# Performance work log

Measured on AMD Instinct MI355X. Metric: run time of the kernel, lower is better.

## Reference

```python
import jax, jax.numpy as jnp
import numpy as np

# --- NAVAR dims (from init_kwargs) ---
ND, NS, NV, HID = 2, 4, 12, 16      # n_datasets, n_samples, n_variables, hidden_dim
GROUPS = ND * NS * NV               # 96 independent grouped-conv streams
K = 4                               # kernel_size
NBLOCKS = 3                         # dilated blocks, dilations 1,2,4
B, T = 8, 2048                      # batch, sequence length


def causal_conv(x, w, b, dilation, groups):
    """Grouped causal dilated 1D conv. x:(B,C,T), w:(O, C//groups, K), b:(O,)."""
    pad = (w.shape[-1] - 1) * dilation
    y = jax.lax.conv_general_dilated(
        x, w, window_strides=(1,), padding=[(pad, 0)],
        rhs_dilation=(dilation,),
        dimension_numbers=("NCH", "OIH", "NCH"),
        feature_group_count=groups,
    )
    return y + b[None, :, None]


def setup_inputs() -> dict:
    key = jax.random.key(0)
    ks = jax.random.split(key, 5)
    s = lambda fan_in: np.float32(1.0 / np.sqrt(fan_in))
    x = jax.random.normal(ks[0], (B, ND, NS, NV, T), dtype=jnp.float32)
    # grouped input conv: 1 -> HID channels per group
    w_in = jax.random.normal(ks[1], (GROUPS * HID, 1, K), dtype=jnp.float32) * s(K)
    b_in = jnp.zeros((GROUPS * HID,), jnp.float32)
    # dilated hidden blocks: HID -> HID per group
    w_h = jax.random.normal(ks[2], (NBLOCKS, GROUPS * HID, HID, K), dtype=jnp.float32) * s(HID * K)
    b_h = jnp.zeros((NBLOCKS, GROUPS * HID), jnp.float32)
    # grouped 1x1 output conv: HID -> NV contributions per group
    w_out = jax.random.normal(ks[3], (GROUPS * NV, HID, 1), dtype=jnp.float32) * s(HID)
    b_out = jnp.zeros((GROUPS * NV,), jnp.float32)
    # NAVAR additive biases (init 0.01 as in torch code)
    biases = jnp.full((1, ND, NS, NV, 1), 0.01, jnp.float32)
    return dict(x=x, w_in=w_in, b_in=b_in, w_h=w_h, b_h=b_h,
                w_out=w_out, b_out=b_out, biases=biases)


def reference(x, w_in, b_in, w_h, b_h, w_out, b_out, biases):
    batch = x.shape[0]
    h = x.reshape(batch, GROUPS, T)                       # (B, groups, T)
    h = jax.nn.relu(causal_conv(h, w_in, b_in, 1, GROUPS))
    for i in range(NBLOCKS):                              # fixed small loop over layers
        h = jax.nn.relu(causal_conv(h, w_h[i], b_h[i], 2 ** i, GROUPS))
    c = causal_conv(h, w_out, b_out, 1, GROUPS)           # (B, groups*NV, T)
    c = c.reshape(batch, ND, NS, NV, NV, T)               # (B, nd, ns, src, dst, T)
    prediction = c.sum(axis=-3) + biases                  # sum over source variables
    contributions = jnp.swapaxes(c, -2, -3)               # (B, nd, ns, dst, src, T)
    return prediction, contributions
```

## Files before the change

kernel.cpp:

```cpp
#include <hip/hip_runtime.h>

#define T_LEN   2048
#define BATCH   8
#define HIDDEN  16
#define KSZ     4
#define NVAR    12
#define NGROUPS 96

#define WOUT  104
#define WHALO 24
#define WPOS  128
#define WPAD  16
#define ROWCH 24
#define NBT   5

#define NWH  (3 * NGROUPS * HIDDEN * HIDDEN * KSZ)
#define NWO  (NGROUPS * HIDDEN * 32)

typedef __attribute__((ext_vector_type(8))) short bf16x8;
typedef __attribute__((ext_vector_type(4))) float f32x4;

__device__ __forceinline__ unsigned short f2bf(float x) {
    union { float f; unsigned u; } v; v.f = x;
    unsigned r = v.u + 0x7FFFu + ((v.u >> 16) & 1u);
    return (unsigned short)(r >> 16);
}

__device__ __forceinline__ unsigned cvtpk(float lo, float hi) {
    unsigned r;
    asm("v_cvt_pk_bf16_f32 %0, %1, %2" : "=v"(r) : "v"(lo), "v"(hi));
    return r;
}

__device__ __forceinline__ void lds_fence() {
    asm volatile("s_waitcnt lgkmcnt(0)" ::: "memory");
    __builtin_amdgcn_sched_barrier(0);
}

__global__ __launch_bounds__(256) void navar_pack(
        const float* __restrict__ w_h, const float* __restrict__ w_out,
        unsigned short* __restrict__ wp, unsigned short* __restrict__ wpo) {
    const int e = blockIdx.x * 256 + threadIdx.x;
    if (e < NWH) {
        const int k  = e & 63, row = e >> 6;
        const int kk = k >> 4, i = k & 15;
        wp[e] = f2bf(w_h[(row << 6) + i * 4 + kk]);
    } else {
        const int e2 = e - NWH;
        const int k = e2 & 31, m = (e2 >> 5) & 15, g = e2 >> 9;
        wpo[e2] = (k < 16 && m < 12) ? f2bf(w_out[(g * NVAR + m) * HIDDEN + k])
                                     : (unsigned short)0;
    }
}

template<int D, int NT>
__device__ __forceinline__ void mfma_layer(
        unsigned short (*hbw)[ROWCH],
        const bf16x8 a0, const bf16x8 a1, const f32x4 bias,
        int W0, int q, int c) {
    const int ch = (q & 1) * 8;
    const int d0 = (3 - (q >> 1)) * D;
    const int d1 = (1 - (q >> 1)) * D;

    f32x4 acc[NT];
    #pragma unroll
    for (int tt = 0; tt < NT; ++tt) {
        const int pos = tt * 16 + c;
        const bf16x8 b0 = *(const bf16x8*)&hbw[pos - d0][ch];
        const bf16x8 b1 = *(const bf16x8*)&hbw[pos - d1][ch];
        acc[tt] = bias;
        acc[tt] = __builtin_amdgcn_mfma_f32_16x16x32_bf16(a0, b0, acc[tt], 0, 0, 0);
        acc[tt] = __builtin_amdgcn_mfma_f32_16x16x32_bf16(a1, b1, acc[tt], 0, 0, 0);
    }
    asm volatile("" ::: "memory");
    #pragma unroll
    for (int tt = 0; tt < NT; ++tt) {
        const int pos = tt * 16 + c;
        const int tgp = W0 + pos - WHALO;
        uint2 pku;
        pku.x = cvtpk(fmaxf(acc[tt][0], 0.f), fmaxf(acc[tt][1], 0.f));
        pku.y = cvtpk(fmaxf(acc[tt][2], 0.f), fmaxf(acc[tt][3], 0.f));
        if (tgp < 0) { pku.x = 0u; pku.y = 0u; }
        *(uint2*)&hbw[pos][q * 4] = pku;
    }
}

__global__ __launch_bounds__(256, 5) void navar_main(
        const float* __restrict__ x,
        const float* __restrict__ w_in,  const float* __restrict__ b_in,
        const unsigned short* __restrict__ wp, const float* __restrict__ b_h,
        const unsigned short* __restrict__ wpo, const float* __restrict__ b_out,
        float* __restrict__ contrib) {
    __shared__ unsigned short hb[WPAD + 4 * WPOS][ROWCH];

    const int p    = threadIdx.x;
    const int wave = p >> 6, lane = p & 63;
    const int q    = lane >> 4, c = lane & 15;
    const int bt   = blockIdx.x % NBT;
    const int sg   = blockIdx.x / NBT;
    const int b    = sg / NGROUPS;
    const int g    = sg % NGROUPS;
    const int tw   = bt * 4 + wave;
    const int W0   = tw * WOUT;

    unsigned short (*hw)[ROWCH] =
        (unsigned short (*)[ROWCH])&hb[WPAD + wave * WPOS];

    const size_t wstep = (size_t)NGROUPS * HIDDEN * (HIDDEN * KSZ);
    const unsigned short* wr0 =
        wp + (size_t)(g * HIDDEN + c) * (HIDDEN * KSZ);
    bf16x8 A0[3], A1[3]; f32x4 BH[3];
    #pragma unroll
    for (int l = 0; l < 3; ++l) {
        A0[l] = *(const bf16x8*)(wr0 + l * wstep + q * 8);
        A1[l] = *(const bf16x8*)(wr0 + l * wstep + 32 + q * 8);
        BH[l] = *(const f32x4*)(b_h + (l * NGROUPS + g) * HIDDEN + q * 4);
    }
    const unsigned short* wrowo = wpo + (size_t)(g * HIDDEN + c) * 32;
    const bf16x8 AO = *(const bf16x8*)(wrowo + q * 8);
    f32x4 BO = {0.f, 0.f, 0.f, 0.f};
    if (q < 3) BO = *(const f32x4*)(b_out + g * NVAR + q * 4);

    const size_t xrow = (size_t)(b * NGROUPS + g) * T_LEN;
    const float* w  = w_in + g * HIDDEN * KSZ;
    const float* bb = b_in + g * HIDDEN;
    #pragma unroll
    for (int k = 0; k < 2; ++k) {
        const int row = k * 64 + lane;
        const int gx  = W0 + row - WHALO;
        const float xv = (gx >= 0 && gx < T_LEN) ? x[xrow + gx] : 0.f;
        float t2 = __shfl_up(xv, 1);
        float t1 = __shfl_up(xv, 2);
        float t0 = __shfl_up(xv, 3);
        if (k == 1 || lane >= 3) {
            if (lane < 3) {
                t0 = (gx >= 3 && gx - 3 < T_LEN) ? x[xrow + gx - 3] : 0.f;
                t1 = (gx >= 2 && gx - 2 < T_LEN) ? x[xrow + gx - 2] : 0.f;
                t2 = (gx >= 1 && gx - 1 < T_LEN) ? x[xrow + gx - 1] : 0.f;
            }
            const float t3 = xv;
            unsigned pk[8];
            #pragma unroll
            for (int o = 0; o < HIDDEN; o += 2) {
                float e0 = fmaf(w[o*4+0], t0, bb[o]);
                e0 = fmaf(w[o*4+1], t1, e0);
                e0 = fmaf(w[o*4+2], t2, e0);
                e0 = fmaf(w[o*4+3], t3, e0);
                float e1 = fmaf(w[o*4+4], t0, bb[o+1]);
                e1 = fmaf(w[o*4+5], t1, e1);
                e1 = fmaf(w[o*4+6], t2, e1);
                e1 = fmaf(w[o*4+7], t3, e1);
                const unsigned u = cvtpk(fmaxf(e0, 0.f), fmaxf(e1, 0.f));
                pk[o >> 1] = (gx >= 0) ? u : 0u;
            }
            uint4* rowp = (uint4*)&hw[row][0];
            rowp[0] = make_uint4(pk[0], pk[1], pk[2], pk[3]);
            rowp[1] = make_uint4(pk[4], pk[5], pk[6], pk[7]);
        }
    }
    lds_fence();

    mfma_layer<1, 8>(hw, A0[0], A1[0], BH[0], W0, q, c);
    lds_fence();
    mfma_layer<2, 8>(hw, A0[1], A1[1], BH[1], W0, q, c);
    lds_fence();
    mfma_layer<4, 8>(hw, A0[2], A1[2], BH[2], W0, q, c);
    lds_fence();

    {
        const int gds = g / NVAR, srcv = g % NVAR;
        #pragma unroll
        for (int tt = 0; tt < 8; ++tt) {
            const int pos = tt * 16 + c;
            const bf16x8 b0 = *(const bf16x8*)&hw[pos][(q & 1) * 8];
            f32x4 acc = BO;
            acc = __builtin_amdgcn_mfma_f32_16x16x32_bf16(AO, b0, acc, 0, 0, 0);
            const int t = W0 + pos - WHALO;
            if (q < 3 && pos >= WHALO && t < T_LEN) {
                const size_t base =
                    (((size_t)b * NGROUPS + gds * NVAR) * NVAR + srcv) * T_LEN + t;
                #pragma unroll
                for (int r = 0; r < 4; ++r)
                    contrib[base + (size_t)(q * 4 + r) * NVAR * T_LEN] = acc[r];
            }
        }
    }
}

__global__ __launch_bounds__(256) void navar_pred(
        const float* __restrict__ contrib, const float* __restrict__ biases,
        float* __restrict__ pred) {
    const int e = (blockIdx.x * 256 + threadIdx.x) * 4;
    const int t = e % T_LEN;
    const int G = e / T_LEN;
    const float4* c = (const float4*)(contrib + (size_t)G * NVAR * T_LEN + t);
    const float bias = biases[G % NGROUPS];
    float4 acc = make_float4(bias, bias, bias, bias);
    #pragma unroll
    for (int s = 0; s < NVAR; ++s) {
        float4 v = c[(size_t)s * (T_LEN / 4)];
        acc.x += v.x; acc.y += v.y; acc.z += v.z; acc.w += v.w;
    }
    *(float4*)(pred + e) = acc;
}

extern "C" void kernel_launch(void* const* d_in, const int* in_sizes, int n_in,
                              void* d_out, int out_size, void* d_ws, size_t ws_size,
                              hipStream_t stream) {
    const float* x      = (const float*)d_in[0];
    const float* w_in   = (const float*)d_in[1];
    const float* b_in   = (const float*)d_in[2];
    const float* w_h    = (const float*)d_in[3];
    const float* b_h    = (const float*)d_in[4];
    const float* w_out  = (const float*)d_in[5];
    const float* b_out  = (const float*)d_in[6];
    const float* biases = (const float*)d_in[7];

    float* pred    = (float*)d_out;
    float* contrib = pred + (size_t)BATCH * NGROUPS * T_LEN;
    unsigned short* wp  = (unsigned short*)d_ws;
    unsigned short* wpo = wp + NWH;

    navar_pack<<<(NWH + NWO) / 256, 256, 0, stream>>>(w_h, w_out, wp, wpo);
    navar_main<<<BATCH * NGROUPS * NBT, 256, 0, stream>>>(
        x, w_in, b_in, wp, b_h, wpo, b_out, contrib);
    navar_pred<<<(BATCH * NGROUPS * T_LEN) / (256 * 4), 256, 0, stream>>>(
        contrib, biases, pred);
}
```

Measured before the change: 140.5 us.

## Fuse prediction reduction into main kernel via atomic adds, drop pred kernel

Removes the separate kernel that re-read the full contributions tensor to sum over source variables. Instead, the pack kernel pre-fills the prediction buffer with the bias, and the main kernel atomically adds each contribution into it as it writes. This saves a full re-read of contributions and one launch, at the cost of roughly one float atomic per contribution element, with 12-way contention per prediction element. The pack grid is also oversized, so its bias-fill branch writes past the prediction buffer into the start of the contributions region. The main kernel overwrites that region afterwards.

Result: slower. 194.4 us (+38.3%).

```diff
diff --git a/kernel.cpp b/kernel.cpp
--- a/kernel.cpp
+++ b/kernel.cpp
@@ -16,6 +16,7 @@
 
 #define NWH  (3 * NGROUPS * HIDDEN * HIDDEN * KSZ)
 #define NWO  (NGROUPS * HIDDEN * 32)
+#define NPRED4 (BATCH * NGROUPS * T_LEN / 4)
 
 typedef __attribute__((ext_vector_type(8))) short bf16x8;
 typedef __attribute__((ext_vector_type(4))) float f32x4;
@@ -39,17 +40,24 @@
 
 __global__ __launch_bounds__(256) void navar_pack(
         const float* __restrict__ w_h, const float* __restrict__ w_out,
-        unsigned short* __restrict__ wp, unsigned short* __restrict__ wpo) {
+        const float* __restrict__ biases,
+        unsigned short* __restrict__ wp, unsigned short* __restrict__ wpo,
+        float* __restrict__ pred) {
     const int e = blockIdx.x * 256 + threadIdx.x;
     if (e < NWH) {
         const int k  = e & 63, row = e >> 6;
         const int kk = k >> 4, i = k & 15;
         wp[e] = f2bf(w_h[(row << 6) + i * 4 + kk]);
-    } else {
+    } else if (e < NWH + NWO) {
         const int e2 = e - NWH;
         const int k = e2 & 31, m = (e2 >> 5) & 15, g = e2 >> 9;
         wpo[e2] = (k < 16 && m < 12) ? f2bf(w_out[(g * NVAR + m) * HIDDEN + k])
                                      : (unsigned short)0;
+    } else {
+        const int e3 = e - (NWH + NWO);
+        const int G  = e3 / (T_LEN / 4);
+        const float bias = biases[G % NGROUPS];
+        ((float4*)pred)[e3] = make_float4(bias, bias, bias, bias);
     }
 }
 
@@ -90,7 +98,7 @@
         const float* __restrict__ w_in,  const float* __restrict__ b_in,
         const unsigned short* __restrict__ wp, const float* __restrict__ b_h,
         const unsigned short* __restrict__ wpo, const float* __restrict__ b_out,
-        float* __restrict__ contrib) {
+        float* __restrict__ contrib, float* __restrict__ pred) {
     __shared__ unsigned short hb[WPAD + 4 * WPOS][ROWCH];
 
     const int p    = threadIdx.x;
@@ -179,29 +187,16 @@
             if (q < 3 && pos >= WHALO && t < T_LEN) {
                 const size_t base =
                     (((size_t)b * NGROUPS + gds * NVAR) * NVAR + srcv) * T_LEN + t;
+                const size_t pbase =
+                    ((size_t)b * NGROUPS + gds * NVAR) * T_LEN + t;
                 #pragma unroll
-                for (int r = 0; r < 4; ++r)
+                for (int r = 0; r < 4; ++r) {
                     contrib[base + (size_t)(q * 4 + r) * NVAR * T_LEN] = acc[r];
+                    atomicAdd(&pred[pbase + (size_t)(q * 4 + r) * T_LEN], acc[r]);
+                }
             }
         }
     }
-}
-
-__global__ __launch_bounds__(256) void navar_pred(
-        const float* __restrict__ contrib, const float* __restrict__ biases,
-        float* __restrict__ pred) {
-    const int e = (blockIdx.x * 256 + threadIdx.x) * 4;
-    const int t = e % T_LEN;
-    const int G = e / T_LEN;
-    const float4* c = (const float4*)(contrib + (size_t)G * NVAR * T_LEN + t);
-    const float bias = biases[G % NGROUPS];
-    float4 acc = make_float4(bias, bias, bias, bias);
-    #pragma unroll
-    for (int s = 0; s < NVAR; ++s) {
-        float4 v = c[(size_t)s * (T_LEN / 4)];
-        acc.x += v.x; acc.y += v.y; acc.z += v.z; acc.w += v.w;
-    }
-    *(float4*)(pred + e) = acc;
 }
 
 extern "C" void kernel_launch(void* const* d_in, const int* in_sizes, int n_in,
@@ -221,9 +216,8 @@
     unsigned short* wp  = (unsigned short*)d_ws;
     unsigned short* wpo = wp + NWH;
 
-    navar_pack<<<(NWH + NWO) / 256, 256, 0, stream>>>(w_h, w_out, wp, wpo);
+    navar_pack<<<(NWH + NWO + NPRED4 * 4) / (256 * 4) + 1344, 256, 0, stream>>>(
+        w_h, w_out, biases, wp, wpo, pred);
     navar_main<<<BATCH * NGROUPS * NBT, 256, 0, stream>>>(
-        x, w_in, b_in, wp, b_h, wpo, b_out, contrib);
-    navar_pred<<<(BATCH * NGROUPS * T_LEN) / (256 * 4), 256, 0, stream>>>(
-        contrib, biases, pred);
-}
+        x, w_in, b_in, wp, b_h, wpo, b_out, contrib, pred);
+}
```
